# Kernel tuning notes

Measured on AMD Instinct MI355X. Metric: run time of the kernel, lower is better.

## Reference

```python
import jax, jax.numpy as jnp
import numpy as np

NUM_NODES = 100000
NUM_EDGES = 1600000
NUM_GRAPHS = 64
IN_DIM = 128
HID = 128
OUT_DIM = 256
NUM_LAYERS = 5
BN_EPS = 1e-5


def _bn(t, gamma, beta):
    # BatchNorm1d forward with batch statistics (biased variance), as in train mode
    m = jnp.mean(t, axis=0)
    v = jnp.var(t, axis=0)
    return gamma * (t - m) * jax.lax.rsqrt(v + BN_EPS) + beta


def setup_inputs() -> dict:
    key = jax.random.key(0)
    ks = jax.random.split(key, 16)
    x = jax.random.normal(ks[0], (NUM_NODES, IN_DIM), dtype=jnp.float32)
    edge_index = jax.random.randint(ks[1], (2, NUM_EDGES), 0, NUM_NODES, dtype=jnp.int64)
    batch = jnp.sort(jax.random.randint(ks[2], (NUM_NODES,), 0, NUM_GRAPHS, dtype=jnp.int64))
    s1 = 1.0 / np.sqrt(IN_DIM)
    s2 = 1.0 / np.sqrt(HID)
    # stacked per-layer GIN MLP params: Linear(HID,HID) -> BN -> ReLU -> Linear(HID,HID)
    w1 = jax.random.normal(ks[3], (NUM_LAYERS, HID, HID), dtype=jnp.float32) * s1
    b1 = jnp.zeros((NUM_LAYERS, HID), dtype=jnp.float32)
    gamma1 = jnp.ones((NUM_LAYERS, HID), dtype=jnp.float32)
    beta1 = jnp.zeros((NUM_LAYERS, HID), dtype=jnp.float32)
    w2 = jax.random.normal(ks[4], (NUM_LAYERS, HID, HID), dtype=jnp.float32) * s2
    b2 = jnp.zeros((NUM_LAYERS, HID), dtype=jnp.float32)
    # outer per-layer BatchNorm after each GINConv
    gamma_bn = jnp.ones((NUM_LAYERS, HID), dtype=jnp.float32)
    beta_bn = jnp.zeros((NUM_LAYERS, HID), dtype=jnp.float32)
    # output projection Linear(HID, OUT_DIM)
    wp = jax.random.normal(ks[5], (HID, OUT_DIM), dtype=jnp.float32) * s2
    bp = jnp.zeros((OUT_DIM,), dtype=jnp.float32)
    return {"x": x, "edge_index": edge_index, "batch": batch,
            "w1": w1, "b1": b1, "gamma1": gamma1, "beta1": beta1,
            "w2": w2, "b2": b2, "gamma_bn": gamma_bn, "beta_bn": beta_bn,
            "wp": wp, "bp": bp}


def reference(x, edge_index, batch, w1, b1, gamma1, beta1, w2, b2, gamma_bn, beta_bn, wp, bp):
    src, dst = edge_index[0], edge_index[1]
    h = x
    for i in range(NUM_LAYERS):
        # GINConv, eps=0: mlp((1+eps)*h + sum_{j in N(i)} h_j)
        agg = jax.ops.segment_sum(h[src], dst, num_segments=NUM_NODES)
        z = h + agg
        t = _bn(z @ w1[i] + b1[i], gamma1[i], beta1[i])
        t = jax.nn.relu(t)
        t = t @ w2[i] + b2[i]
        # outer BatchNorm + ReLU (dropout p handled as identity in eval)
        t = jax.nn.relu(_bn(t, gamma_bn[i], beta_bn[i]))
        h = h + t  # residual (dims always match)
    node_emb = h
    # global mean pool per graph
    sums = jax.ops.segment_sum(h, batch, num_segments=NUM_GRAPHS)
    counts = jax.ops.segment_sum(jnp.ones((NUM_NODES,), dtype=h.dtype), batch, num_segments=NUM_GRAPHS)
    pooled = sums / jnp.maximum(counts, 1.0)[:, None]
    graph_emb = pooled @ wp + bp
    return graph_emb, node_emb
```

## Files before the change

kernel.cpp:

```cpp
#include <hip/hip_runtime.h>

#define NNODES 100000
#define NEDGES 1600000
#define NGRAPHS 64
#define HID 128
#define OUTD 256
#define NLAYERS 5
#define BN_EPS 1e-5f
#define NBUCK 196
#define BUCKCAP 9216
#define FILL_BLOCKS 391
#define NREP1 64
#define NREP2 8

typedef __attribute__((ext_vector_type(8))) short short8;
typedef __attribute__((ext_vector_type(4))) float f32x4;

__device__ inline unsigned short f2b(float f) {
    union { float f; unsigned int u; } a; a.f = f;
    unsigned int u = a.u;
    return (unsigned short)((u + 0x7FFF + ((u >> 16) & 1)) >> 16);
}
__device__ inline float b2f(unsigned short b) {
    union { unsigned int u; float f; } a; a.u = ((unsigned int)b) << 16;
    return a.f;
}

union U8 { short8 v; unsigned short u[8]; };

__global__ void k_init(const float* __restrict__ x, float* __restrict__ h,
                       ushort* __restrict__ hb,
                       const float* __restrict__ w1, const float* __restrict__ w2,
                       unsigned short* __restrict__ WT, int* __restrict__ bcur) {
    int b = blockIdx.x;
    if (b < 12500) {
        int i = b * 256 + threadIdx.x;
        float4 v = ((const float4*)x)[i];
        ((float4*)h)[i] = v;
        ushort4 o;
        o.x = f2b(v.x); o.y = f2b(v.y); o.z = f2b(v.z); o.w = f2b(v.w);
        ((ushort4*)hb)[i] = o;
    } else {
        int t = (b - 12500) * 256 + threadIdx.x;
        int mat = t >> 14;
        int rem = t & 16383;
        int k = rem >> 7, n = rem & 127;
        const float* src = (mat < 5) ? &w1[(size_t)mat * 16384]
                                     : &w2[(size_t)(mat - 5) * 16384];
        WT[(size_t)mat * 16384 + n * 128 + k] = f2b(src[k * 128 + n]);
        if (b == 12500 && threadIdx.x < NBUCK)
            bcur[threadIdx.x] = threadIdx.x * BUCKCAP;
    }
}

__global__ __launch_bounds__(256) void k_fill1(
    const int* __restrict__ srcv, const int* __restrict__ dstv,
    int* __restrict__ bcur, unsigned int* __restrict__ packed) {
    __shared__ int hist[NBUCK];
    __shared__ int base[NBUCK];
    int tid = threadIdx.x;
    int e0 = blockIdx.x * 4096;
    for (int i = tid; i < NBUCK; i += 256) hist[i] = 0;
    __syncthreads();
#pragma unroll
    for (int i = 0; i < 16; i++) {
        int e = e0 + i * 256 + tid;
        if (e < NEDGES) atomicAdd(&hist[dstv[e] >> 9], 1);
    }
    __syncthreads();
    for (int i = tid; i < NBUCK; i += 256) {
        int c = hist[i];
        base[i] = c ? atomicAdd(&bcur[i], c) : 0;
        hist[i] = 0;
    }
    __syncthreads();
#pragma unroll
    for (int i = 0; i < 16; i++) {
        int e = e0 + i * 256 + tid;
        if (e < NEDGES) {
            int d = dstv[e];
            int b = d >> 9;
            int r = atomicAdd(&hist[b], 1);
            packed[base[b] + r] = ((unsigned int)srcv[e] << 9) | (unsigned int)(d & 511);
        }
    }
}

__global__ __launch_bounds__(256) void k_fill2(
    const unsigned int* __restrict__ packed, const int* __restrict__ bcur,
    int2* __restrict__ off2, int* __restrict__ adj) {
    __shared__ int deg[512];
    __shared__ int cur[512];
    int tid = threadIdx.x;
    int b = blockIdx.x;
    int base = b * BUCKCAP;
    int cnt = bcur[b] - base;
    deg[tid] = 0; deg[tid + 256] = 0;
    __syncthreads();
    for (int i = tid; i < cnt; i += 256)
        atomicAdd(&deg[packed[base + i] & 511], 1);
    __syncthreads();
    cur[tid] = deg[tid]; cur[tid + 256] = deg[tid + 256];
    __syncthreads();
    for (int o = 1; o < 512; o <<= 1) {
        int u0 = (tid >= o) ? cur[tid - o] : 0;
        int u1 = (tid + 256 >= o) ? cur[tid + 256 - o] : 0;
        __syncthreads();
        cur[tid] += u0; cur[tid + 256] += u1;
        __syncthreads();
    }
    int nbase = b * 512;
#pragma unroll
    for (int i = 0; i < 2; i++) {
        int t = tid + i * 256;
        int st = base + cur[t] - deg[t];
        int n = nbase + t;
        if (n < NNODES) off2[n] = make_int2(st, st + deg[t]);
    }
    __syncthreads();
#pragma unroll
    for (int i = 0; i < 2; i++) {
        int t = tid + i * 256;
        cur[t] = base + cur[t] - deg[t];
    }
    __syncthreads();
    for (int i = tid; i < cnt; i += 256) {
        unsigned int p = packed[base + i];
        int r = atomicAdd(&cur[p & 511], 1);
        adj[r] = (int)(p >> 9);
    }
}

__global__ __launch_bounds__(256) void k_ag1(
    const ushort* __restrict__ hb, const int2* __restrict__ off2,
    const int* __restrict__ adj, const unsigned short* __restrict__ WT,
    const float* __restrict__ bias, ushort* __restrict__ C,
    float* __restrict__ stats) {
    __shared__ ushort zt[16 * 128];
    __shared__ float lstat[256];
    int tid = threadIdx.x;
    int n = tid >> 4;
    int c = tid & 15;
    int node = blockIdx.x * 16 + n;
    const short8* hb8 = (const short8*)hb;

    U8 sv; sv.v = hb8[(size_t)node * 16 + c];
    float acc[8];
#pragma unroll
    for (int k = 0; k < 8; k++) acc[k] = b2f(sv.u[k]);

    int2 oo = off2[node];
    int e = oo.x, e1 = oo.y;
    for (; e + 8 <= e1; e += 8) {
        int s[8];
#pragma unroll
        for (int j = 0; j < 8; j++) s[j] = adj[e + j];
        U8 u[8];
#pragma unroll
        for (int j = 0; j < 8; j++) u[j].v = hb8[(size_t)s[j] * 16 + c];
#pragma unroll
        for (int j = 0; j < 8; j++)
#pragma unroll
            for (int k = 0; k < 8; k++) acc[k] += b2f(u[j].u[k]);
    }
    for (; e + 4 <= e1; e += 4) {
        int s0 = adj[e], s1 = adj[e + 1], s2 = adj[e + 2], s3 = adj[e + 3];
        U8 u0, u1, u2, u3;
        u0.v = hb8[(size_t)s0 * 16 + c];
        u1.v = hb8[(size_t)s1 * 16 + c];
        u2.v = hb8[(size_t)s2 * 16 + c];
        u3.v = hb8[(size_t)s3 * 16 + c];
#pragma unroll
        for (int k = 0; k < 8; k++)
            acc[k] += (b2f(u0.u[k]) + b2f(u1.u[k])) + (b2f(u2.u[k]) + b2f(u3.u[k]));
    }
    for (; e < e1; e++) {
        int s = adj[e];
        U8 u; u.v = hb8[(size_t)s * 16 + c];
#pragma unroll
        for (int k = 0; k < 8; k++) acc[k] += b2f(u.u[k]);
    }

    U8 o;
#pragma unroll
    for (int k = 0; k < 8; k++) o.u[k] = f2b(acc[k]);
    *(short8*)((char*)zt + ((n * 256 + c * 16) ^ ((n & 7) << 4))) = o.v;
    __syncthreads();

    int wave = tid >> 6;
    int lane = tid & 63;
    int q = lane >> 4;
    int l16 = lane & 15;

    f32x4 gacc[2];
    gacc[0] = (f32x4){0.f, 0.f, 0.f, 0.f};
    gacc[1] = (f32x4){0.f, 0.f, 0.f, 0.f};

#pragma unroll
    for (int kc = 0; kc < 4; kc++) {
        int k0 = kc * 32 + q * 8;
        int ch = kc * 4 + q;
        short8 av = *(const short8*)(
            (char*)zt + ((l16 * 256 + ch * 16) ^ ((l16 & 7) << 4)));
#pragma unroll
        for (int nt = 0; nt < 2; nt++) {
            int col0 = (wave * 2 + nt) * 16;
            short8 bf = *(const short8*)&WT[(size_t)(col0 + l16) * 128 + k0];
            gacc[nt] = __builtin_amdgcn_mfma_f32_16x16x32_bf16(
                av, bf, gacc[nt], 0, 0, 0);
        }
    }

    int rowbase = blockIdx.x * 16;
#pragma unroll
    for (int nt = 0; nt < 2; nt++) {
        int col = (wave * 2 + nt) * 16 + l16;
        float b = bias[col];
        float csum = 0.f, csq = 0.f;
#pragma unroll
        for (int r = 0; r < 4; r++) {
            int row = rowbase + q * 4 + r;
            float v = gacc[nt][r] + b;
            C[(size_t)row * 128 + col] = f2b(v);
            csum += v; csq += v * v;
        }
        csum += __shfl_xor(csum, 16, 64); csq += __shfl_xor(csq, 16, 64);
        csum += __shfl_xor(csum, 32, 64); csq += __shfl_xor(csq, 32, 64);
        if (q == 0) { lstat[col] = csum; lstat[128 + col] = csq; }
    }
    __syncthreads();
    atomicAdd(&stats[((blockIdx.x & (NREP1 - 1)) << 8) + tid], lstat[tid]);
}

__global__ __launch_bounds__(256) void k_gemm2(
    const ushort* __restrict__ A, const unsigned short* __restrict__ WT,
    const float* __restrict__ bias, ushort* __restrict__ C,
    const float* __restrict__ statsIn, const float* __restrict__ gamma,
    const float* __restrict__ beta, float* __restrict__ stats) {
    __shared__ float lstat[256];
    __shared__ float s_sc[128], s_sh[128];
    int tid = threadIdx.x;
    if (tid < 128) {
        float s = 0.f, qq = 0.f;
#pragma unroll
        for (int r = 0; r < NREP1; r++) {
            s  += statsIn[r * 256 + tid];
            qq += statsIn[r * 256 + 128 + tid];
        }
        float m = s * (1.f / NNODES);
        float var = qq * (1.f / NNODES) - m * m;
        float sc = gamma[tid] * rsqrtf(var + BN_EPS);
        s_sc[tid] = sc;
        s_sh[tid] = beta[tid] - m * sc;
    }
    __syncthreads();

    int wave = tid >> 6;
    int lane = tid & 63;
    int q = lane >> 4;
    int l16 = lane & 15;
    int rowbase = blockIdx.x * 128 + wave * 32;

    f32x4 acc[2][8];
#pragma unroll
    for (int rt = 0; rt < 2; rt++)
#pragma unroll
        for (int nt = 0; nt < 8; nt++) acc[rt][nt] = (f32x4){0.f, 0.f, 0.f, 0.f};

    for (int kc = 0; kc < 4; kc++) {
        int k0 = kc * 32 + q * 8;
        short8 bf[8];
#pragma unroll
        for (int nt = 0; nt < 8; nt++)
            bf[nt] = *(const short8*)&WT[(size_t)(nt * 16 + l16) * 128 + k0];

        float4 s0 = *(const float4*)&s_sc[k0];
        float4 s1 = *(const float4*)&s_sc[k0 + 4];
        float4 t0 = *(const float4*)&s_sh[k0];
        float4 t1 = *(const float4*)&s_sh[k0 + 4];
        float scl[8] = {s0.x, s0.y, s0.z, s0.w, s1.x, s1.y, s1.z, s1.w};
        float shf[8] = {t0.x, t0.y, t0.z, t0.w, t1.x, t1.y, t1.z, t1.w};
#pragma unroll
        for (int rt = 0; rt < 2; rt++) {
            int row = rowbase + rt * 16 + l16;
            if (row >= NNODES) row = NNODES - 1;
            union { short8 s; unsigned short u[8]; } in, cv;
            in.s = *(const short8*)&A[(size_t)row * 128 + k0];
#pragma unroll
            for (int j = 0; j < 8; j++) {
                float f = fmaxf(b2f(in.u[j]) * scl[j] + shf[j], 0.f);
                cv.u[j] = f2b(f);
            }
#pragma unroll
            for (int nt = 0; nt < 8; nt++)
                acc[rt][nt] = __builtin_amdgcn_mfma_f32_16x16x32_bf16(
                    cv.s, bf[nt], acc[rt][nt], 0, 0, 0);
        }
    }

    lstat[tid] = 0.f;
    __syncthreads();
#pragma unroll
    for (int nt = 0; nt < 8; nt++) {
        float b = bias[nt * 16 + l16];
        float csum = 0.f, csq = 0.f;
#pragma unroll
        for (int rt = 0; rt < 2; rt++) {
            int rb = rowbase + rt * 16 + q * 4;
#pragma unroll
            for (int r = 0; r < 4; r++) {
                int row = rb + r;
                if (row < NNODES) {
                    float v = acc[rt][nt][r] + b;
                    C[(size_t)row * 128 + nt * 16 + l16] = f2b(v);
                    csum += v; csq += v * v;
                }
            }
        }
        csum += __shfl_xor(csum, 16, 64); csq += __shfl_xor(csq, 16, 64);
        csum += __shfl_xor(csum, 32, 64); csq += __shfl_xor(csq, 32, 64);
        if (q == 0) {
            atomicAdd(&lstat[nt * 16 + l16], csum);
            atomicAdd(&lstat[128 + nt * 16 + l16], csq);
        }
    }
    __syncthreads();
    atomicAdd(&stats[((blockIdx.x & (NREP2 - 1)) << 8) + tid], lstat[tid]);
}

__global__ void k_resid(float* __restrict__ h, ushort* __restrict__ hb,
                        const ushort* __restrict__ t2b,
                        const float* __restrict__ statsIn,
                        const float* __restrict__ gamma, const float* __restrict__ beta) {
    __shared__ float s_sc[128], s_sh[128];
    int tid = threadIdx.x;
    if (tid < 128) {
        float s = 0.f, qq = 0.f;
#pragma unroll
        for (int r = 0; r < NREP2; r++) {
            s  += statsIn[r * 256 + tid];
            qq += statsIn[r * 256 + 128 + tid];
        }
        float m = s * (1.f / NNODES);
        float var = qq * (1.f / NNODES) - m * m;
        float sc = gamma[tid] * rsqrtf(var + BN_EPS);
        s_sc[tid] = sc;
        s_sh[tid] = beta[tid] - m * sc;
    }
    __syncthreads();
    int i = blockIdx.x * 256 + tid;
    int c4 = (i & 31) * 4;
    float4 sc = *(const float4*)&s_sc[c4];
    float4 sh = *(const float4*)&s_sh[c4];
    ushort4 t = ((const ushort4*)t2b)[i];
    float4 hv = ((float4*)h)[i];
    hv.x += fmaxf(b2f(t.x) * sc.x + sh.x, 0.f);
    hv.y += fmaxf(b2f(t.y) * sc.y + sh.y, 0.f);
    hv.z += fmaxf(b2f(t.z) * sc.z + sh.z, 0.f);
    hv.w += fmaxf(b2f(t.w) * sc.w + sh.w, 0.f);
    ((float4*)h)[i] = hv;
    ushort4 o;
    o.x = f2b(hv.x); o.y = f2b(hv.y); o.z = f2b(hv.z); o.w = f2b(hv.w);
    ((ushort4*)hb)[i] = o;
}

__global__ void k_pool(const float* __restrict__ h, const int* __restrict__ batch,
                       float* __restrict__ pooled, float* __restrict__ gcnt) {
    __shared__ float4 red[256];
    __shared__ int lcnt[NGRAPHS];
    int t = threadIdx.x;
    int d4 = t & 31, sub = t >> 5;
    int n0 = blockIdx.x * 128;
    if (n0 >= NNODES) return;
    int n1 = n0 + 128; if (n1 > NNODES) n1 = NNODES;
    if (t < NGRAPHS) lcnt[t] = 0;
    __syncthreads();
    if (t < n1 - n0) atomicAdd(&lcnt[batch[n0 + t]], 1);
    __syncthreads();
    if (t < NGRAPHS && lcnt[t]) atomicAdd(&gcnt[t], (float)lcnt[t]);

    int glo = batch[n0], ghi = batch[n1 - 1];
    for (int g = glo; g <= ghi; g++) {
        float4 acc = make_float4(0.f, 0.f, 0.f, 0.f);
        for (int r = n0 + sub; r < n1; r += 8) {
            if (batch[r] == g) {
                float4 v = ((const float4*)h)[(size_t)r * 32 + d4];
                acc.x += v.x; acc.y += v.y; acc.z += v.z; acc.w += v.w;
            }
        }
        red[t] = acc;
        __syncthreads();
        if (sub < 4) {
            float4 o = red[t + 128];
            red[t].x += o.x; red[t].y += o.y; red[t].z += o.z; red[t].w += o.w;
        }
        __syncthreads();
        if (sub < 2) {
            float4 o = red[t + 64];
            red[t].x += o.x; red[t].y += o.y; red[t].z += o.z; red[t].w += o.w;
        }
        __syncthreads();
        if (sub == 0) {
            float4 o = red[t + 32];
            float4 a = red[t];
            a.x += o.x; a.y += o.y; a.z += o.z; a.w += o.w;
            atomicAdd(&pooled[g * 128 + d4 * 4 + 0], a.x);
            atomicAdd(&pooled[g * 128 + d4 * 4 + 1], a.y);
            atomicAdd(&pooled[g * 128 + d4 * 4 + 2], a.z);
            atomicAdd(&pooled[g * 128 + d4 * 4 + 3], a.w);
        }
        __syncthreads();
    }
}

__global__ void k_proj(const float* __restrict__ pooled, const float* __restrict__ cnt,
                       const float* __restrict__ wp, const float* __restrict__ bp,
                       float* __restrict__ out) {
    __shared__ float prow[128];
    int g = blockIdx.x, c = threadIdx.x;
    if (c < 128) prow[c] = pooled[g * 128 + c] / fmaxf(cnt[g], 1.f);
    __syncthreads();
    float acc = bp[c];
    for (int k = 0; k < 128; k++) acc += prow[k] * wp[k * 256 + c];
    out[g * 256 + c] = acc;
}

extern "C" void kernel_launch(void* const* d_in, const int* in_sizes, int n_in,
                              void* d_out, int out_size, void* d_ws, size_t ws_size,
                              hipStream_t stream) {
    const float* x    = (const float*)d_in[0];
    const int*   eidx = (const int*)d_in[1];
    const int*   batch= (const int*)d_in[2];
    const float* w1   = (const float*)d_in[3];
    const float* b1   = (const float*)d_in[4];
    const float* g1   = (const float*)d_in[5];
    const float* be1  = (const float*)d_in[6];
    const float* w2   = (const float*)d_in[7];
    const float* b2   = (const float*)d_in[8];
    const float* gbn  = (const float*)d_in[9];
    const float* bbn  = (const float*)d_in[10];
    const float* wp   = (const float*)d_in[11];
    const float* bp   = (const float*)d_in[12];

    float* out  = (float*)d_out;
    float* gemb = out;
    float* h    = out + (size_t)NGRAPHS * OUTD;

    char* w = (char*)d_ws;
    ushort* hb   = (ushort*)w; w += (size_t)NNODES * 128 * 2;
    ushort* t2b  = (ushort*)w; w += (size_t)NNODES * 128 * 2;
    ushort* tb   = (ushort*)w; w += (size_t)NNODES * 128 * 2;
    int2*  off2  = (int2*)w;  w += (size_t)NNODES * 8;
    int*   adj   = (int*)w;   w += (size_t)NBUCK * BUCKCAP * 4;
    unsigned short* WT = (unsigned short*)w; w += (size_t)10 * 16384 * 2;
    int*   bcur  = (int*)w;   w += 256 * 4;
    float* statsAll = (float*)w; w += (size_t)NLAYERS * (NREP1 + NREP2) * 256 * 4;
    float* pooled= (float*)w; w += (size_t)NGRAPHS * HID * 4;
    float* gcnt  = (float*)w; w += NGRAPHS * 4;

    unsigned int* packed = (unsigned int*)tb;

    const int* srcv = eidx;
    const int* dstv = eidx + NEDGES;

    k_init<<<12500 + 640, 256, 0, stream>>>(x, h, hb, w1, w2, WT, bcur);

    hipMemsetAsync(statsAll, 0,
                   ((size_t)NLAYERS * (NREP1 + NREP2) * 256 + NGRAPHS * HID + NGRAPHS) * 4,
                   stream);

    k_fill1<<<FILL_BLOCKS, 256, 0, stream>>>(srcv, dstv, bcur, packed);
    k_fill2<<<NBUCK, 256, 0, stream>>>(packed, bcur, off2, adj);

    for (int i = 0; i < NLAYERS; i++) {
        float* st1 = statsAll + (size_t)i * (NREP1 + NREP2) * 256;
        float* st2 = st1 + (size_t)NREP1 * 256;
        k_ag1<<<NNODES / 16, 256, 0, stream>>>(
            hb, off2, adj, WT + (size_t)i * 16384, b1 + i * HID, tb, st1);
        k_gemm2<<<(NNODES + 127) / 128, 256, 0, stream>>>(
            tb, WT + (size_t)(5 + i) * 16384, b2 + i * HID, t2b,
            st1, g1 + i * HID, be1 + i * HID, st2);
        k_resid<<<NNODES * 128 / 4 / 256, 256, 0, stream>>>(
            h, hb, t2b, st2, gbn + i * HID, bbn + i * HID);
    }

    k_pool<<<(NNODES + 127) / 128, 256, 0, stream>>>(h, batch, pooled, gcnt);
    k_proj<<<NGRAPHS, 256, 0, stream>>>(pooled, gcnt, wp, bp, gemb);
}
```

Measured before the change: 946.3 us.

## Replace replicated atomic BN stats with per-block partials and separate reduction kernel

Each block of the aggregation and second GEMM kernels now writes its BN partial sums to a dedicated row instead of atomically adding into a small replicated array. A new reduction kernel folds these rows into a single stats vector that the consumer kernels read directly. The residual kernel also processes eight float4 chunks per thread with fewer blocks, and the GEMM k-loop is fully unrolled. The aim is to remove global atomic contention, at the cost of two extra kernel launches per layer and extra partial-buffer traffic.

```diff
diff --git a/kernel.cpp b/kernel.cpp
--- a/kernel.cpp
+++ b/kernel.cpp
@@ -10,8 +10,9 @@
 #define NBUCK 196
 #define BUCKCAP 9216
 #define FILL_BLOCKS 391
-#define NREP1 64
-#define NREP2 8
+#define AG1B 6250
+#define G2B 782
+#define RESB 1563
 
 typedef __attribute__((ext_vector_type(8))) short short8;
 typedef __attribute__((ext_vector_type(4))) float f32x4;
@@ -135,7 +136,7 @@
     const ushort* __restrict__ hb, const int2* __restrict__ off2,
     const int* __restrict__ adj, const unsigned short* __restrict__ WT,
     const float* __restrict__ bias, ushort* __restrict__ C,
-    float* __restrict__ stats) {
+    float* __restrict__ raw1) {
     __shared__ ushort zt[16 * 128];
     __shared__ float lstat[256];
     int tid = threadIdx.x;
@@ -229,30 +230,36 @@
         if (q == 0) { lstat[col] = csum; lstat[128 + col] = csq; }
     }
     __syncthreads();
-    atomicAdd(&stats[((blockIdx.x & (NREP1 - 1)) << 8) + tid], lstat[tid]);
+    raw1[(size_t)blockIdx.x * 256 + tid] = lstat[tid];
+}
+
+__global__ __launch_bounds__(256) void k_red(const float* __restrict__ raw,
+                                             float* __restrict__ stc, int nrows) {
+    int t = threadIdx.x;
+    float s = 0.f;
+    for (int r = blockIdx.x; r < nrows; r += gridDim.x)
+        s += raw[(size_t)r * 256 + t];
+    atomicAdd(&stc[t], s);
 }
 
 __global__ __launch_bounds__(256) void k_gemm2(
     const ushort* __restrict__ A, const unsigned short* __restrict__ WT,
     const float* __restrict__ bias, ushort* __restrict__ C,
-    const float* __restrict__ statsIn, const float* __restrict__ gamma,
-    const float* __restrict__ beta, float* __restrict__ stats) {
+    const float* __restrict__ st1c, const float* __restrict__ gamma,
+    const float* __restrict__ beta, float* __restrict__ raw2) {
     __shared__ float lstat[256];
     __shared__ float s_sc[128], s_sh[128];
     int tid = threadIdx.x;
     if (tid < 128) {
-        float s = 0.f, qq = 0.f;
-#pragma unroll
-        for (int r = 0; r < NREP1; r++) {
-            s  += statsIn[r * 256 + tid];
-            qq += statsIn[r * 256 + 128 + tid];
-        }
+        float s  = st1c[tid];
+        float qq = st1c[128 + tid];
         float m = s * (1.f / NNODES);
         float var = qq * (1.f / NNODES) - m * m;
         float sc = gamma[tid] * rsqrtf(var + BN_EPS);
         s_sc[tid] = sc;
         s_sh[tid] = beta[tid] - m * sc;
     }
+    lstat[tid] = 0.f;
     __syncthreads();
 
     int wave = tid >> 6;
@@ -267,6 +274,7 @@
 #pragma unroll
         for (int nt = 0; nt < 8; nt++) acc[rt][nt] = (f32x4){0.f, 0.f, 0.f, 0.f};
 
+#pragma unroll
     for (int kc = 0; kc < 4; kc++) {
         int k0 = kc * 32 + q * 8;
         short8 bf[8];
@@ -298,8 +306,6 @@
         }
     }
 
-    lstat[tid] = 0.f;
-    __syncthreads();
 #pragma unroll
     for (int nt = 0; nt < 8; nt++) {
         float b = bias[nt * 16 + l16];
@@ -325,22 +331,18 @@
         }
     }
     __syncthreads();
-    atomicAdd(&stats[((blockIdx.x & (NREP2 - 1)) << 8) + tid], lstat[tid]);
-}
-
-__global__ void k_resid(float* __restrict__ h, ushort* __restrict__ hb,
-                        const ushort* __restrict__ t2b,
-                        const float* __restrict__ statsIn,
-                        const float* __restrict__ gamma, const float* __restrict__ beta) {
+    raw2[(size_t)blockIdx.x * 256 + tid] = lstat[tid];
+}
+
+__global__ __launch_bounds__(256) void k_resid(
+    float* __restrict__ h, ushort* __restrict__ hb,
+    const ushort* __restrict__ t2b, const float* __restrict__ st2c,
+    const float* __restrict__ gamma, const float* __restrict__ beta) {
     __shared__ float s_sc[128], s_sh[128];
     int tid = threadIdx.x;
     if (tid < 128) {
-        float s = 0.f, qq = 0.f;
-#pragma unroll
-        for (int r = 0; r < NREP2; r++) {
-            s  += statsIn[r * 256 + tid];
-            qq += statsIn[r * 256 + 128 + tid];
-        }
+        float s  = st2c[tid];
+        float qq = st2c[128 + tid];
         float m = s * (1.f / NNODES);
         float var = qq * (1.f / NNODES) - m * m;
         float sc = gamma[tid] * rsqrtf(var + BN_EPS);
@@ -348,20 +350,25 @@
         s_sh[tid] = beta[tid] - m * sc;
     }
     __syncthreads();
-    int i = blockIdx.x * 256 + tid;
-    int c4 = (i & 31) * 4;
-    float4 sc = *(const float4*)&s_sc[c4];
-    float4 sh = *(const float4*)&s_sh[c4];
-    ushort4 t = ((const ushort4*)t2b)[i];
-    float4 hv = ((float4*)h)[i];
-    hv.x += fmaxf(b2f(t.x) * sc.x + sh.x, 0.f);
-    hv.y += fmaxf(b2f(t.y) * sc.y + sh.y, 0.f);
-    hv.z += fmaxf(b2f(t.z) * sc.z + sh.z, 0.f);
-    hv.w += fmaxf(b2f(t.w) * sc.w + sh.w, 0.f);
-    ((float4*)h)[i] = hv;
-    ushort4 o;
-    o.x = f2b(hv.x); o.y = f2b(hv.y); o.z = f2b(hv.z); o.w = f2b(hv.w);
-    ((ushort4*)hb)[i] = o;
+#pragma unroll
+    for (int it = 0; it < 8; it++) {
+        int i = blockIdx.x * 2048 + it * 256 + tid;
+        if (i < NNODES * 32) {
+            int c4 = (i & 31) * 4;
+            float4 sc = *(const float4*)&s_sc[c4];
+            float4 sh = *(const float4*)&s_sh[c4];
+            ushort4 t = ((const ushort4*)t2b)[i];
+            float4 hv = ((float4*)h)[i];
+            hv.x += fmaxf(b2f(t.x) * sc.x + sh.x, 0.f);
+            hv.y += fmaxf(b2f(t.y) * sc.y + sh.y, 0.f);
+            hv.z += fmaxf(b2f(t.z) * sc.z + sh.z, 0.f);
+            hv.w += fmaxf(b2f(t.w) * sc.w + sh.w, 0.f);
+            ((float4*)h)[i] = hv;
+            ushort4 o;
+            o.x = f2b(hv.x); o.y = f2b(hv.y); o.z = f2b(hv.z); o.w = f2b(hv.w);
+            ((ushort4*)hb)[i] = o;
+        }
+    }
 }
 
 __global__ void k_pool(const float* __restrict__ h, const int* __restrict__ batch,
@@ -454,7 +461,9 @@
     int*   adj   = (int*)w;   w += (size_t)NBUCK * BUCKCAP * 4;
     unsigned short* WT = (unsigned short*)w; w += (size_t)10 * 16384 * 2;
     int*   bcur  = (int*)w;   w += 256 * 4;
-    float* statsAll = (float*)w; w += (size_t)NLAYERS * (NREP1 + NREP2) * 256 * 4;
+    float* raw1  = (float*)w; w += (size_t)AG1B * 256 * 4;
+    float* raw2  = (float*)w; w += (size_t)G2B * 256 * 4;
+    float* stc   = (float*)w; w += (size_t)NLAYERS * 512 * 4;
     float* pooled= (float*)w; w += (size_t)NGRAPHS * HID * 4;
     float* gcnt  = (float*)w; w += NGRAPHS * 4;
 
@@ -465,23 +474,24 @@
 
     k_init<<<12500 + 640, 256, 0, stream>>>(x, h, hb, w1, w2, WT, bcur);
 
-    hipMemsetAsync(statsAll, 0,
-                   ((size_t)NLAYERS * (NREP1 + NREP2) * 256 + NGRAPHS * HID + NGRAPHS) * 4,
-                   stream);
+    hipMemsetAsync(stc, 0,
+                   ((size_t)NLAYERS * 512 + NGRAPHS * HID + NGRAPHS) * 4, stream);
 
     k_fill1<<<FILL_BLOCKS, 256, 0, stream>>>(srcv, dstv, bcur, packed);
     k_fill2<<<NBUCK, 256, 0, stream>>>(packed, bcur, off2, adj);
 
     for (int i = 0; i < NLAYERS; i++) {
-        float* st1 = statsAll + (size_t)i * (NREP1 + NREP2) * 256;
-        float* st2 = st1 + (size_t)NREP1 * 256;
-        k_ag1<<<NNODES / 16, 256, 0, stream>>>(
-            hb, off2, adj, WT + (size_t)i * 16384, b1 + i * HID, tb, st1);
-        k_gemm2<<<(NNODES + 127) / 128, 256, 0, stream>>>(
+        float* st1c = stc + (size_t)i * 512;
+        float* st2c = st1c + 256;
+        k_ag1<<<AG1B, 256, 0, stream>>>(
+            hb, off2, adj, WT + (size_t)i * 16384, b1 + i * HID, tb, raw1);
+        k_red<<<64, 256, 0, stream>>>(raw1, st1c, AG1B);
+        k_gemm2<<<G2B, 256, 0, stream>>>(
             tb, WT + (size_t)(5 + i) * 16384, b2 + i * HID, t2b,
-            st1, g1 + i * HID, be1 + i * HID, st2);
-        k_resid<<<NNODES * 128 / 4 / 256, 256, 0, stream>>>(
-            h, hb, t2b, st2, gbn + i * HID, bbn + i * HID);
+            st1c, g1 + i * HID, be1 + i * HID, raw2);
+        k_red<<<8, 256, 0, stream>>>(raw2, st2c, G2B);
+        k_resid<<<RESB, 256, 0, stream>>>(
+            h, hb, t2b, st2c, gbn + i * HID, bbn + i * HID);
     }
 
     k_pool<<<(NNODES + 127) / 128, 256, 0, stream>>>(h, batch, pooled, gcnt);
```

New measurement: 1.191 ms. 25.8% more time.
